# Optimization experiments

Hardware: AMD Instinct MI355X
Metric: run time of the kernel (lower is better)

## Reference

```python
import jax, jax.numpy as jnp
import numpy as np

B, V, L = 256, 128000, 2048
EPS = 1e-05


def setup_inputs() -> dict:
    key = jax.random.key(0)
    k1, k2, k3, k4, k5 = jax.random.split(key, 5)
    logits_next = jax.random.normal(k1, (B, V), jnp.float32)
    token_ids = jax.random.randint(k2, (B, L), 0, V, jnp.int32)
    presence_penalties = jax.random.uniform(k3, (B,), jnp.float32) * 1.5
    temperatures = jax.random.uniform(k4, (B,), jnp.float32, 0.5, 1.5)
    # make first quarter of the batch greedy (temperature == 0)
    temperatures = temperatures.at[: B // 4].set(0.0)
    u = jax.random.uniform(k5, (B, V), jnp.float32, 1e-9, 1.0)
    gumbel = -jnp.log(-jnp.log(u))  # Gumbel(0,1) noise for multinomial sampling
    return {
        "logits_next": logits_next,
        "token_ids": token_ids,
        "presence_penalties": presence_penalties,
        "temperatures": temperatures,
        "gumbel": gumbel,
    }


def reference(logits_next, token_ids, presence_penalties, temperatures, gumbel):
    Bn, Vn = logits_next.shape
    # presence mask: 1.0 where token id appeared in the history (counts > 0)
    rows = jnp.arange(Bn, dtype=jnp.int32)[:, None]  # [B,1]
    presence = jnp.zeros((Bn, Vn), logits_next.dtype).at[rows, token_ids].set(1.0)
    penalized = logits_next - presence_penalties[:, None] * presence

    greedy = temperatures < EPS  # [B]
    safe_t = jnp.where(greedy, jnp.float32(1.0), temperatures)
    scaled = penalized / safe_t[:, None]

    # greedy rows: plain argmax; sample rows: Gumbel-max == multinomial(softmax)
    greedy_tok = jnp.argmax(penalized, axis=-1)
    sampled_tok = jnp.argmax(scaled + gumbel, axis=-1)
    token_ids_next = jnp.where(greedy, greedy_tok, sampled_tok)
    return token_ids_next.astype(jnp.int32)
```

## Files before the change

kernel.cpp:

```cpp
#include <hip/hip_runtime.h>
#include <math.h>

#define BATCH 256
#define VOCAB 128000
#define HIST  2048
#define EPS_T 1e-5f

#define BLOCK 1024
#define NWAVES (BLOCK / 64)
#define MASK_WORDS (VOCAB / 32)

__global__ __launch_bounds__(BLOCK) void sampler_kernel(
    const float* __restrict__ logits,
    const int*   __restrict__ token_ids,
    const float* __restrict__ penalties,
    const float* __restrict__ temps,
    const float* __restrict__ gumbel,
    int*         __restrict__ out)
{
    __shared__ unsigned int mask[MASK_WORDS];
    __shared__ float wval[NWAVES];
    __shared__ int   widx[NWAVES];

    const int b   = blockIdx.x;
    const int tid = threadIdx.x;

    for (int i = tid; i < MASK_WORDS; i += BLOCK) mask[i] = 0u;
    __syncthreads();

    const int* row_tok = token_ids + (size_t)b * HIST;
    for (int i = tid; i < HIST; i += BLOCK) {
        int t = row_tok[i];
        atomicOr(&mask[t >> 5], 1u << (t & 31));
    }
    __syncthreads();

    const float pen    = penalties[b];
    const float temp   = temps[b];
    const bool  greedy = (temp < EPS_T);

    float best  = -INFINITY;
    int   besti = 0x7fffffff;

    const float4* lg = (const float4*)(logits + (size_t)b * VOCAB);
    const float4* gm = (const float4*)(gumbel + (size_t)b * VOCAB);
    const int nvec = VOCAB / 4;

    if (greedy) {
        for (int i = tid; i < nvec; i += BLOCK) {
            float4 l = lg[i];
            const int v = i * 4;
            const unsigned w = mask[v >> 5];
            const int sh = v & 31;
            float lv[4] = {l.x, l.y, l.z, l.w};
            #pragma unroll
            for (int j = 0; j < 4; j++) {
                float present = (float)((w >> (sh + j)) & 1u);
                float p = lv[j] - pen * present;
                int idx = v + j;
                if (p > best || (p == best && idx < besti)) { best = p; besti = idx; }
            }
        }
    } else {
        for (int i = tid; i < nvec; i += BLOCK) {
            float4 l = lg[i];
            float4 g = gm[i];
            const int v = i * 4;
            const unsigned w = mask[v >> 5];
            const int sh = v & 31;
            float lv[4] = {l.x, l.y, l.z, l.w};
            float gv[4] = {g.x, g.y, g.z, g.w};
            #pragma unroll
            for (int j = 0; j < 4; j++) {
                float present = (float)((w >> (sh + j)) & 1u);
                float p = lv[j] - pen * present;
                float s = p / temp + gv[j];
                int idx = v + j;
                if (s > best || (s == best && idx < besti)) { best = s; besti = idx; }
            }
        }
    }

    #pragma unroll
    for (int off = 32; off > 0; off >>= 1) {
        float ov = __shfl_down(best, off, 64);
        int   oi = __shfl_down(besti, off, 64);
        if (ov > best || (ov == best && oi < besti)) { best = ov; besti = oi; }
    }

    const int wave = tid >> 6;
    const int lane = tid & 63;
    if (lane == 0) { wval[wave] = best; widx[wave] = besti; }
    __syncthreads();

    if (tid == 0) {
        #pragma unroll
        for (int wv = 1; wv < NWAVES; wv++) {
            if (wval[wv] > best || (wval[wv] == best && widx[wv] < besti)) {
                best = wval[wv]; besti = widx[wv];
            }
        }
        out[b] = besti;
    }
}

extern "C" void kernel_launch(void* const* d_in, const int* in_sizes, int n_in,
                              void* d_out, int out_size, void* d_ws, size_t ws_size,
                              hipStream_t stream) {
    const float* logits    = (const float*)d_in[0];
    const int*   token_ids = (const int*)d_in[1];
    const float* penalties = (const float*)d_in[2];
    const float* temps     = (const float*)d_in[3];
    const float* gumbel    = (const float*)d_in[4];
    int* out = (int*)d_out;

    sampler_kernel<<<BATCH, BLOCK, 0, stream>>>(logits, token_ids, penalties,
                                                temps, gumbel, out);
}
```

Baseline: 275.1 us.

## Split each vocab row across four blocks with a second reduction kernel

Each batch row is now handled by four blocks, each covering a quarter of the vocabulary with its own smaller presence bitmask. Per-segment partial argmax results go to workspace, and a tiny second kernel combines them. The main loop is also unrolled to issue four float4 loads per thread at once, giving more memory-level parallelism. In exchange, every segment block re-reads the full token history, and there is an extra kernel launch.

```diff
diff --git a/kernel.cpp b/kernel.cpp
--- a/kernel.cpp
+++ b/kernel.cpp
@@ -8,30 +8,44 @@
 
 #define BLOCK 1024
 #define NWAVES (BLOCK / 64)
-#define MASK_WORDS (VOCAB / 32)
 
-__global__ __launch_bounds__(BLOCK) void sampler_kernel(
+#define SEGS 4
+#define SEG_ELEMS (VOCAB / SEGS)
+#define SEG_VEC   (SEG_ELEMS / 4)
+#define SEG_WORDS (SEG_ELEMS / 32)
+
+__device__ __forceinline__ void upd(float s, int idx, float& best, int& besti) {
+    if (s > best || (s == best && idx < besti)) { best = s; besti = idx; }
+}
+
+__global__ __launch_bounds__(BLOCK) void sampler_partial_kernel(
     const float* __restrict__ logits,
     const int*   __restrict__ token_ids,
     const float* __restrict__ penalties,
     const float* __restrict__ temps,
     const float* __restrict__ gumbel,
-    int*         __restrict__ out)
+    float*       __restrict__ pvals,
+    int*         __restrict__ pidxs)
 {
-    __shared__ unsigned int mask[MASK_WORDS];
+    __shared__ unsigned int smask[SEG_WORDS];
     __shared__ float wval[NWAVES];
     __shared__ int   widx[NWAVES];
 
-    const int b   = blockIdx.x;
+    const int blk = blockIdx.x;
+    const int b   = blk >> 2;
+    const int seg = blk & 3;
     const int tid = threadIdx.x;
 
-    for (int i = tid; i < MASK_WORDS; i += BLOCK) mask[i] = 0u;
+    if (tid < SEG_WORDS) smask[tid] = 0u;
     __syncthreads();
 
+    const int tok_lo = seg * SEG_ELEMS;
+    const int tok_hi = tok_lo + SEG_ELEMS;
     const int* row_tok = token_ids + (size_t)b * HIST;
     for (int i = tid; i < HIST; i += BLOCK) {
         int t = row_tok[i];
-        atomicOr(&mask[t >> 5], 1u << (t & 31));
+        if (t >= tok_lo && t < tok_hi)
+            atomicOr(&smask[(t - tok_lo) >> 5], 1u << (t & 31));
     }
     __syncthreads();
 
@@ -42,41 +56,79 @@
     float best  = -INFINITY;
     int   besti = 0x7fffffff;
 
-    const float4* lg = (const float4*)(logits + (size_t)b * VOCAB);
-    const float4* gm = (const float4*)(gumbel + (size_t)b * VOCAB);
-    const int nvec = VOCAB / 4;
+    const float4* lg = (const float4*)(logits + (size_t)b * VOCAB) + (size_t)seg * SEG_VEC;
+    const float4* gm = (const float4*)(gumbel + (size_t)b * VOCAB) + (size_t)seg * SEG_VEC;
+    const int abs_base = seg * SEG_ELEMS;
 
     if (greedy) {
-        for (int i = tid; i < nvec; i += BLOCK) {
-            float4 l = lg[i];
-            const int v = i * 4;
-            const unsigned w = mask[v >> 5];
-            const int sh = v & 31;
-            float lv[4] = {l.x, l.y, l.z, l.w};
+        int iv = tid;
+        for (; iv + 3 * BLOCK < SEG_VEC; iv += 4 * BLOCK) {
+            float4 l[4];
+            #pragma unroll
+            for (int k = 0; k < 4; k++) l[k] = lg[iv + k * BLOCK];
+            #pragma unroll
+            for (int k = 0; k < 4; k++) {
+                const int lv = iv + k * BLOCK;
+                const unsigned w = smask[lv >> 3];
+                const int sh = (lv * 4) & 31;
+                float e[4] = {l[k].x, l[k].y, l[k].z, l[k].w};
+                #pragma unroll
+                for (int j = 0; j < 4; j++) {
+                    float present = (float)((w >> (sh + j)) & 1u);
+                    float p = e[j] - pen * present;
+                    upd(p, abs_base + lv * 4 + j, best, besti);
+                }
+            }
+        }
+        for (; iv < SEG_VEC; iv += BLOCK) {
+            float4 l = lg[iv];
+            const unsigned w = smask[iv >> 3];
+            const int sh = (iv * 4) & 31;
+            float e[4] = {l.x, l.y, l.z, l.w};
             #pragma unroll
             for (int j = 0; j < 4; j++) {
                 float present = (float)((w >> (sh + j)) & 1u);
-                float p = lv[j] - pen * present;
-                int idx = v + j;
-                if (p > best || (p == best && idx < besti)) { best = p; besti = idx; }
+                float p = e[j] - pen * present;
+                upd(p, abs_base + iv * 4 + j, best, besti);
             }
         }
     } else {
-        for (int i = tid; i < nvec; i += BLOCK) {
-            float4 l = lg[i];
-            float4 g = gm[i];
-            const int v = i * 4;
-            const unsigned w = mask[v >> 5];
-            const int sh = v & 31;
-            float lv[4] = {l.x, l.y, l.z, l.w};
+        int iv = tid;
+        for (; iv + 3 * BLOCK < SEG_VEC; iv += 4 * BLOCK) {
+            float4 l[4], g[4];
+            #pragma unroll
+            for (int k = 0; k < 4; k++) l[k] = lg[iv + k * BLOCK];
+            #pragma unroll
+            for (int k = 0; k < 4; k++) g[k] = gm[iv + k * BLOCK];
+            #pragma unroll
+            for (int k = 0; k < 4; k++) {
+                const int lv = iv + k * BLOCK;
+                const unsigned w = smask[lv >> 3];
+                const int sh = (lv * 4) & 31;
+                float e[4] = {l[k].x, l[k].y, l[k].z, l[k].w};
+                float gv[4] = {g[k].x, g[k].y, g[k].z, g[k].w};
+                #pragma unroll
+                for (int j = 0; j < 4; j++) {
+                    float present = (float)((w >> (sh + j)) & 1u);
+                    float p = e[j] - pen * present;
+                    float s = p / temp + gv[j];
+                    upd(s, abs_base + lv * 4 + j, best, besti);
+                }
+            }
+        }
+        for (; iv < SEG_VEC; iv += BLOCK) {
+            float4 l = lg[iv];
+            float4 g = gm[iv];
+            const unsigned w = smask[iv >> 3];
+            const int sh = (iv * 4) & 31;
+            float e[4] = {l.x, l.y, l.z, l.w};
             float gv[4] = {g.x, g.y, g.z, g.w};
             #pragma unroll
             for (int j = 0; j < 4; j++) {
                 float present = (float)((w >> (sh + j)) & 1u);
-                float p = lv[j] - pen * present;
+                float p = e[j] - pen * present;
                 float s = p / temp + gv[j];
-                int idx = v + j;
-                if (s > best || (s == best && idx < besti)) { best = s; besti = idx; }
+                upd(s, abs_base + iv * 4 + j, best, besti);
             }
         }
     }
@@ -100,8 +152,24 @@
                 best = wval[wv]; besti = widx[wv];
             }
         }
-        out[b] = besti;
+        pvals[b * SEGS + seg] = best;
+        pidxs[b * SEGS + seg] = besti;
     }
+}
+
+__global__ void sampler_reduce_kernel(const float* __restrict__ pvals,
+                                      const int*   __restrict__ pidxs,
+                                      int*         __restrict__ out)
+{
+    const int b = threadIdx.x;
+    float best  = pvals[b * SEGS];
+    int   besti = pidxs[b * SEGS];
+    #pragma unroll
+    for (int s = 1; s < SEGS; s++) {
+        float v = pvals[b * SEGS + s];
+        if (v > best) { best = v; besti = pidxs[b * SEGS + s]; }
+    }
+    out[b] = besti;
 }
 
 extern "C" void kernel_launch(void* const* d_in, const int* in_sizes, int n_in,
@@ -114,6 +182,10 @@
     const float* gumbel    = (const float*)d_in[4];
     int* out = (int*)d_out;
 
-    sampler_kernel<<<BATCH, BLOCK, 0, stream>>>(logits, token_ids, penalties,
-                                                temps, gumbel, out);
+    float* pvals = (float*)d_ws;
+    int*   pidxs = (int*)((float*)d_ws + BATCH * SEGS);
+
+    sampler_partial_kernel<<<BATCH * SEGS, BLOCK, 0, stream>>>(
+        logits, token_ids, penalties, temps, gumbel, pvals, pidxs);
+    sampler_reduce_kernel<<<1, BATCH, 0, stream>>>(pvals, pidxs, out);
 }
```

Measured after the change: 272.5 us. No clear change (-0.9%).

## Split sampler into mask build, segmented vocab scan, and final reduce kernels

Applied to the files above, without the earlier changes.

Splits the single per-row kernel into three kernels. The first builds the presence bitmask per row and writes it to workspace. The second splits each row's vocabulary into 25 segments, one block each, with all loads issued up front in registers. The third reduces the per-segment argmax results. This raises the number of blocks from 256 to 6400, so more memory traffic is in flight, at the cost of two extra launches and a global round trip for the mask.

```diff
diff --git a/kernel.cpp b/kernel.cpp
--- a/kernel.cpp
+++ b/kernel.cpp
@@ -6,77 +6,108 @@
 #define HIST  2048
 #define EPS_T 1e-5f
 
-#define BLOCK 1024
-#define NWAVES (BLOCK / 64)
-#define MASK_WORDS (VOCAB / 32)
+#define MASK_WORDS_ROW (VOCAB / 32)
 
-__global__ __launch_bounds__(BLOCK) void sampler_kernel(
+#define ABLOCK 256
+
+#define SEGS 25
+#define SEG_ELEMS (VOCAB / SEGS)
+#define SEG_VEC   (SEG_ELEMS / 4)
+#define SEG_WORDS (SEG_ELEMS / 32)
+#define BBLOCK 256
+#define PAIRS (SEG_VEC / BBLOCK)
+#define BWAVES (BBLOCK / 64)
+
+__global__ __launch_bounds__(ABLOCK) void mask_kernel(
+    const int* __restrict__ token_ids,
+    unsigned int* __restrict__ gmask)
+{
+    __shared__ unsigned int m[MASK_WORDS_ROW];
+    const int b = blockIdx.x, tid = threadIdx.x;
+
+    for (int i = tid; i < MASK_WORDS_ROW; i += ABLOCK) m[i] = 0u;
+    __syncthreads();
+
+    const int* rt = token_ids + (size_t)b * HIST;
+    #pragma unroll
+    for (int k = 0; k < HIST / ABLOCK; k++) {
+        int t = rt[tid + k * ABLOCK];
+        atomicOr(&m[t >> 5], 1u << (t & 31));
+    }
+    __syncthreads();
+
+    unsigned int* gr = gmask + (size_t)b * MASK_WORDS_ROW;
+    for (int i = tid; i < MASK_WORDS_ROW; i += ABLOCK) gr[i] = m[i];
+}
+
+__device__ __forceinline__ void upd(float s, int idx, float& best, int& besti) {
+    if (s > best || (s == best && idx < besti)) { best = s; besti = idx; }
+}
+
+__global__ __launch_bounds__(BBLOCK) void scan_kernel(
     const float* __restrict__ logits,
-    const int*   __restrict__ token_ids,
+    const float* __restrict__ gumbel,
+    const unsigned int* __restrict__ gmask,
     const float* __restrict__ penalties,
     const float* __restrict__ temps,
-    const float* __restrict__ gumbel,
-    int*         __restrict__ out)
+    float* __restrict__ pvals,
+    int*   __restrict__ pidxs)
 {
-    __shared__ unsigned int mask[MASK_WORDS];
-    __shared__ float wval[NWAVES];
-    __shared__ int   widx[NWAVES];
+    __shared__ float wval[BWAVES];
+    __shared__ int   widx[BWAVES];
 
-    const int b   = blockIdx.x;
+    const int blk = blockIdx.x;
+    const int b   = blk / SEGS;
+    const int seg = blk - b * SEGS;
     const int tid = threadIdx.x;
-
-    for (int i = tid; i < MASK_WORDS; i += BLOCK) mask[i] = 0u;
-    __syncthreads();
-
-    const int* row_tok = token_ids + (size_t)b * HIST;
-    for (int i = tid; i < HIST; i += BLOCK) {
-        int t = row_tok[i];
-        atomicOr(&mask[t >> 5], 1u << (t & 31));
-    }
-    __syncthreads();
 
     const float pen    = penalties[b];
     const float temp   = temps[b];
     const bool  greedy = (temp < EPS_T);
 
+    const float4*       lg = (const float4*)(logits + (size_t)b * VOCAB) + seg * SEG_VEC;
+    const float4*       gm = (const float4*)(gumbel + (size_t)b * VOCAB) + seg * SEG_VEC;
+    const unsigned int* mw = gmask + (size_t)b * MASK_WORDS_ROW + seg * SEG_WORDS;
+
+    float4 l[PAIRS];
+    unsigned int w[PAIRS];
+    #pragma unroll
+    for (int k = 0; k < PAIRS; k++) l[k] = lg[tid + k * BBLOCK];
+    #pragma unroll
+    for (int k = 0; k < PAIRS; k++) w[k] = mw[k * (BBLOCK / 8) + (tid >> 3)];
+
     float best  = -INFINITY;
     int   besti = 0x7fffffff;
-
-    const float4* lg = (const float4*)(logits + (size_t)b * VOCAB);
-    const float4* gm = (const float4*)(gumbel + (size_t)b * VOCAB);
-    const int nvec = VOCAB / 4;
+    const int sh = (tid * 4) & 31;
+    const int abs0 = seg * SEG_ELEMS;
 
     if (greedy) {
-        for (int i = tid; i < nvec; i += BLOCK) {
-            float4 l = lg[i];
-            const int v = i * 4;
-            const unsigned w = mask[v >> 5];
-            const int sh = v & 31;
-            float lv[4] = {l.x, l.y, l.z, l.w};
+        #pragma unroll
+        for (int k = 0; k < PAIRS; k++) {
+            const int lv = tid + k * BBLOCK;
+            float e[4] = {l[k].x, l[k].y, l[k].z, l[k].w};
             #pragma unroll
             for (int j = 0; j < 4; j++) {
-                float present = (float)((w >> (sh + j)) & 1u);
-                float p = lv[j] - pen * present;
-                int idx = v + j;
-                if (p > best || (p == best && idx < besti)) { best = p; besti = idx; }
+                float present = (float)((w[k] >> (sh + j)) & 1u);
+                float p = e[j] - pen * present;
+                upd(p, abs0 + lv * 4 + j, best, besti);
             }
         }
     } else {
-        for (int i = tid; i < nvec; i += BLOCK) {
-            float4 l = lg[i];
-            float4 g = gm[i];
-            const int v = i * 4;
-            const unsigned w = mask[v >> 5];
-            const int sh = v & 31;
-            float lv[4] = {l.x, l.y, l.z, l.w};
-            float gv[4] = {g.x, g.y, g.z, g.w};
+        float4 g[PAIRS];
+        #pragma unroll
+        for (int k = 0; k < PAIRS; k++) g[k] = gm[tid + k * BBLOCK];
+        #pragma unroll
+        for (int k = 0; k < PAIRS; k++) {
+            const int lv = tid + k * BBLOCK;
+            float e[4]  = {l[k].x, l[k].y, l[k].z, l[k].w};
+            float gv[4] = {g[k].x, g[k].y, g[k].z, g[k].w};
             #pragma unroll
             for (int j = 0; j < 4; j++) {
-                float present = (float)((w >> (sh + j)) & 1u);
-                float p = lv[j] - pen * present;
+                float present = (float)((w[k] >> (sh + j)) & 1u);
+                float p = e[j] - pen * present;
                 float s = p / temp + gv[j];
-                int idx = v + j;
-                if (s > best || (s == best && idx < besti)) { best = s; besti = idx; }
+                upd(s, abs0 + lv * 4 + j, best, besti);
             }
         }
     }
@@ -87,21 +118,35 @@
         int   oi = __shfl_down(besti, off, 64);
         if (ov > best || (ov == best && oi < besti)) { best = ov; besti = oi; }
     }
-
-    const int wave = tid >> 6;
-    const int lane = tid & 63;
+    const int wave = tid >> 6, lane = tid & 63;
     if (lane == 0) { wval[wave] = best; widx[wave] = besti; }
     __syncthreads();
 
     if (tid == 0) {
         #pragma unroll
-        for (int wv = 1; wv < NWAVES; wv++) {
+        for (int wv = 1; wv < BWAVES; wv++) {
             if (wval[wv] > best || (wval[wv] == best && widx[wv] < besti)) {
                 best = wval[wv]; besti = widx[wv];
             }
         }
-        out[b] = besti;
+        pvals[seg * BATCH + b] = best;
+        pidxs[seg * BATCH + b] = besti;
     }
+}
+
+__global__ void reduce_kernel(const float* __restrict__ pvals,
+                              const int*   __restrict__ pidxs,
+                              int*         __restrict__ out)
+{
+    const int b = threadIdx.x;
+    float best  = pvals[b];
+    int   besti = pidxs[b];
+    #pragma unroll
+    for (int s = 1; s < SEGS; s++) {
+        float v = pvals[s * BATCH + b];
+        if (v > best) { best = v; besti = pidxs[s * BATCH + b]; }
+    }
+    out[b] = besti;
 }
 
 extern "C" void kernel_launch(void* const* d_in, const int* in_sizes, int n_in,
@@ -114,6 +159,12 @@
     const float* gumbel    = (const float*)d_in[4];
     int* out = (int*)d_out;
 
-    sampler_kernel<<<BATCH, BLOCK, 0, stream>>>(logits, token_ids, penalties,
-                                                temps, gumbel, out);
+    unsigned int* gmask = (unsigned int*)d_ws;
+    float* pvals = (float*)((char*)d_ws + (size_t)BATCH * MASK_WORDS_ROW * 4);
+    int*   pidxs = (int*)(pvals + SEGS * BATCH);
+
+    mask_kernel<<<BATCH, ABLOCK, 0, stream>>>(token_ids, gmask);
+    scan_kernel<<<BATCH * SEGS, BBLOCK, 0, stream>>>(logits, gumbel, gmask,
+                                                     penalties, temps, pvals, pidxs);
+    reduce_kernel<<<1, BATCH, 0, stream>>>(pvals, pidxs, out);
 }
```

Result: no change. 273.9 us (-0.5%).
